# Performance work log

Hardware: AMD Instinct MI355X
Metric: run time of the kernel (lower is better)

## Reference

```python
import jax, jax.numpy as jnp
import numpy as np

D_MODEL = 1024
N_HEADS = 16
HEAD_DIM = D_MODEL // N_HEADS
D_FF = 4096
EPS = 1e-5


def _layer_norm(x, gamma, beta):
    mu = jnp.mean(x, axis=-1, keepdims=True)
    var = jnp.var(x, axis=-1, keepdims=True)
    return (x - mu) * jax.lax.rsqrt(var + EPS) * gamma + beta


def setup_inputs() -> dict:
    key = jax.random.key(0)
    ks = jax.random.split(key, 16)
    B, T, S = 2, 2048, 2048
    s = 1.0 / np.sqrt(D_MODEL)
    inp = {
        "tgt": jax.random.normal(ks[0], (B, T, D_MODEL), jnp.float32),
        "memory": jax.random.normal(ks[1], (B, S, D_MODEL), jnp.float32),
        "wq": jax.random.normal(ks[2], (D_MODEL, D_MODEL), jnp.float32) * s,
        "bq": jnp.zeros((D_MODEL,), jnp.float32),
        "wk": jax.random.normal(ks[3], (D_MODEL, D_MODEL), jnp.float32) * s,
        "bk": jnp.zeros((D_MODEL,), jnp.float32),
        "wv": jax.random.normal(ks[4], (D_MODEL, D_MODEL), jnp.float32) * s,
        "bv": jnp.zeros((D_MODEL,), jnp.float32),
        "wo": jax.random.normal(ks[5], (D_MODEL, D_MODEL), jnp.float32) * s,
        "bo": jnp.zeros((D_MODEL,), jnp.float32),
        "w1": jax.random.normal(ks[6], (D_MODEL, D_FF), jnp.float32) * s,
        "b1": jnp.zeros((D_FF,), jnp.float32),
        "w2": jax.random.normal(ks[7], (D_FF, D_MODEL), jnp.float32) * (1.0 / np.sqrt(D_FF)),
        "b2": jnp.zeros((D_MODEL,), jnp.float32),
        "g1": jnp.ones((D_MODEL,), jnp.float32),
        "be1": jnp.zeros((D_MODEL,), jnp.float32),
        "g2": jnp.ones((D_MODEL,), jnp.float32),
        "be2": jnp.zeros((D_MODEL,), jnp.float32),
    }
    return inp


def reference(tgt, memory, wq, bq, wk, bk, wv, bv, wo, bo, w1, b1, w2, b2, g1, be1, g2, be2):
    B, T, _ = tgt.shape
    S = memory.shape[1]
    scale = HEAD_DIM ** -0.5
    # projections -> [B, H, L, Dh]
    Q = (tgt @ wq + bq).reshape(B, T, N_HEADS, HEAD_DIM).transpose(0, 2, 1, 3)
    K = (memory @ wk + bk).reshape(B, S, N_HEADS, HEAD_DIM).transpose(0, 2, 1, 3)
    V = (memory @ wv + bv).reshape(B, S, N_HEADS, HEAD_DIM).transpose(0, 2, 1, 3)
    scores = jnp.einsum("bhtd,bhsd->bhts", Q, K) * scale
    attn = jax.nn.softmax(scores, axis=-1)  # dropout=0 (eval)
    ctx = jnp.einsum("bhts,bhsd->bhtd", attn, V)
    ctx = ctx.transpose(0, 2, 1, 3).reshape(B, T, D_MODEL)
    attn_out = ctx @ wo + bo
    # post-norm residual blocks
    x = _layer_norm(tgt + attn_out, g1, be1)
    ff = jax.nn.relu(x @ w1 + b1) @ w2 + b2
    out = _layer_norm(x + ff, g2, be2)
    return out
```

## Files before the change

### kernel.cpp

```cpp
#include <hip/hip_runtime.h>


typedef unsigned short u16;
typedef __attribute__((ext_vector_type(8))) short bvec8;
typedef __attribute__((ext_vector_type(4))) float fvec4;
typedef __attribute__((ext_vector_type(4))) unsigned uvec4;

#define MFMA16(a, b, c) __builtin_amdgcn_mfma_f32_16x16x32_bf16((a), (b), (c), 0, 0, 0)

__device__ __forceinline__ u16 f2b(float f) {
  union { float f; unsigned u; } x; x.f = f;
  unsigned u = x.u;
  return (u16)((u + 0x7FFFu + ((u >> 16) & 1u)) >> 16);
}
__device__ __forceinline__ unsigned cvtpk(float lo, float hi) {
  unsigned r;
  asm("v_cvt_pk_bf16_f32 %0, %1, %2" : "=v"(r) : "v"(lo), "v"(hi));
  return r;
}
#define PLSWAP32(a, b) asm("v_permlane32_swap_b32 %0, %1" : "+v"(a), "+v"(b))
#define PLSWAP16(a, b) asm("v_permlane16_swap_b32 %0, %1" : "+v"(a), "+v"(b))

__device__ __forceinline__ void gl_lds16(const u16* g, u16* lds) {
  __builtin_amdgcn_global_load_lds(
      (const __attribute__((address_space(1))) void*)g,
      (__attribute__((address_space(3))) void*)lds, 16, 0, 0);
}

__global__ __launch_bounds__(256) void k_pre(
    const float* __restrict__ tgt, const float* __restrict__ mem,
    const float* __restrict__ wq, const float* __restrict__ wk,
    const float* __restrict__ wv, const float* __restrict__ wo,
    const float* __restrict__ w1, const float* __restrict__ w2,
    u16* __restrict__ tgt_b, u16* __restrict__ mem_b,
    u16* __restrict__ wqT, u16* __restrict__ wkvT, u16* __restrict__ woT,
    u16* __restrict__ w1T, u16* __restrict__ w2T) {
  __shared__ float t[32][33];
  int bb = blockIdx.x;
  if (bb < 8192) {
    const float* in = (bb < 4096) ? tgt : mem;
    u16* outp = (bb < 4096) ? tgt_b : mem_b;
    int i = (bb & 4095) * 256 + threadIdx.x;
    float4 v = ((const float4*)in)[i];
    ushort4 o;
    o.x = f2b(v.x); o.y = f2b(v.y); o.z = f2b(v.z); o.w = f2b(v.w);
    ((ushort4*)outp)[i] = o;
    return;
  }
  int b = bb - 8192;
  const float* W; u16* WT; int K, N, bx, by;
  if (b < 4096) {
    int m = b >> 10, tt = b & 1023;
    bx = tt & 31; by = tt >> 5; K = 1024; N = 1024;
    W = (m == 0) ? wq : (m == 1) ? wk : (m == 2) ? wv : wo;
    WT = (m == 0) ? wqT : (m == 1) ? wkvT : (m == 2) ? wkvT + 1024 * 1024 : woT;
  } else if (b < 8192) {
    int tt = b - 4096; bx = tt & 127; by = tt >> 7; K = 1024; N = 4096;
    W = w1; WT = w1T;
  } else {
    int tt = b - 8192; bx = tt & 31; by = tt >> 5; K = 4096; N = 1024;
    W = w2; WT = w2T;
  }
  int tx = threadIdx.x & 31, ty = threadIdx.x >> 5;
  int n0 = bx * 32, k0 = by * 32;
#pragma unroll
  for (int i = 0; i < 4; i++)
    t[ty + i * 8][tx] = W[(size_t)(k0 + ty + i * 8) * N + n0 + tx];
  __syncthreads();
#pragma unroll
  for (int i = 0; i < 4; i++)
    WT[(size_t)(n0 + ty + i * 8) * K + k0 + tx] = f2b(t[tx][ty + i * 8]);
}

__global__ __launch_bounds__(256, 4) void k_qkv(
    const u16* __restrict__ tgt_b, const u16* __restrict__ mem_b,
    const u16* __restrict__ wqT, const u16* __restrict__ wkvT,
    const float* __restrict__ bq, const float* __restrict__ bk,
    const float* __restrict__ bv,
    u16* __restrict__ Qb, u16* __restrict__ Kb, u16* __restrict__ Vtb) {
  __shared__ u16 S[256 * 64];
  const int tid = threadIdx.x, w = tid >> 6, lane = tid & 63;
  const int q = lane >> 4, l = lane & 15;
  const bool isQ = blockIdx.x < 256;
  const int pq = isQ ? blockIdx.x : blockIdx.x - 256;
  const int lx = (pq >> 3) & (isQ ? 7 : 15);
  const int ly = (pq & 7) + ((pq >> (isQ ? 6 : 7)) << 3);
  const int m0 = ly * 128, n0 = lx * 128;
  const u16* A = isQ ? tgt_b : mem_b;
  const u16* BT = isQ ? wqT : wkvT;
  const int wm = (w >> 1) * 64, wn = (w & 1) * 64;
  const int rowin = lane >> 3, grp = lane & 7;
  const int gcol = ((grp + rowin) & 7) * 8;
  const int kc0 = ((q + 8 - (l & 7)) & 7) * 8;
  const int kc1 = ((q + 12 - (l & 7)) & 7) * 8;
  const u16* gp[8];
  u16* lp[8];
#pragma unroll
  for (int c = 0; c < 8; c++) {
    int r0 = (w * 8 + c) * 8;
    gp[c] = (r0 < 128) ? A + (size_t)(m0 + r0 + rowin) * 1024 + gcol
                       : BT + (size_t)(n0 + r0 - 128 + rowin) * 1024 + gcol;
    lp[c] = &S[r0 * 64];
  }
  fvec4 acc[4][4] = {};
#pragma unroll 1
  for (int k0 = 0; k0 < 1024; k0 += 64) {
#pragma unroll
    for (int c = 0; c < 8; c++) gl_lds16(gp[c] + k0, lp[c]);
    __syncthreads();
#pragma unroll
    for (int kh = 0; kh < 2; kh++) {
      const int kc = kh ? kc1 : kc0;
      bvec8 af[4], bf[4];
#pragma unroll
      for (int i = 0; i < 4; i++) {
        af[i] = *(const bvec8*)&S[(wm + 16 * i + l) * 64 + kc];
        bf[i] = *(const bvec8*)&S[(128 + wn + 16 * i + l) * 64 + kc];
      }
#pragma unroll
      for (int i = 0; i < 4; i++)
#pragma unroll
        for (int j = 0; j < 4; j++)
          acc[i][j] = MFMA16(af[i], bf[j], acc[i][j]);
    }
    __syncthreads();
  }
#pragma unroll
  for (int mi = 0; mi < 4; mi++)
#pragma unroll
    for (int ni = 0; ni < 4; ni++) {
      int row = m0 + wm + mi * 16 + q * 4;
      int col = n0 + wn + ni * 16 + l;
      if (isQ) {
        float bvv = bq[col];
#pragma unroll
        for (int r = 0; r < 4; r++)
          Qb[(size_t)(row + r) * 1024 + col] = f2b((acc[mi][ni][r] + bvv) * 0.125f);
      } else if (col < 1024) {
        float bvv = bk[col];
#pragma unroll
        for (int r = 0; r < 4; r++)
          Kb[(size_t)(row + r) * 1024 + col] = f2b(acc[mi][ni][r] + bvv);
      } else {
        int vcol = col - 1024;
        float bvv = bv[vcol];
        int b = row >> 11, s = row & 2047;
        int h = vcol >> 6, d = vcol & 63;
        ushort4 o;
        o.x = f2b(acc[mi][ni][0] + bvv);
        o.y = f2b(acc[mi][ni][1] + bvv);
        o.z = f2b(acc[mi][ni][2] + bvv);
        o.w = f2b(acc[mi][ni][3] + bvv);
        *(ushort4*)&Vtb[((size_t)(b * 16 + h) * 64 + d) * 2048 + s] = o;
      }
    }
}

template <int TM, int TN>
__global__ __launch_bounds__(256, 4) void k_gemm(
    const u16* __restrict__ A, const u16* __restrict__ BT,
    const float* __restrict__ bias, const float* __restrict__ resid,
    float* __restrict__ outF, u16* __restrict__ outB,
    int M, int N, int Kstride, int Klen, float scale, int flags) {
  constexpr int WM = TM / 2, WN = TN / 2;
  constexpr int MI = WM / 16, NI = WN / 16;
  constexpr int NCALL = (TM + TN) / 32;
  __shared__ u16 S[(TM + TN) * 64];
  const int tid = threadIdx.x, w = tid >> 6, lane = tid & 63;
  const int q = lane >> 4, l = lane & 15;
  const int nx = gridDim.x, nyh = gridDim.y >> 3;
  const int p = blockIdx.x + nx * (blockIdx.y + gridDim.y * blockIdx.z);
  const int q8 = p >> 3;
  const int lx = q8 & (nx - 1);
  const int t = q8 >> __builtin_ctz(nx);
  const int ly = (p & 7) + ((t & (nyh - 1)) << 3);
  const int lz = t >> __builtin_ctz(nyh);
  const int m0 = ly * TM, n0 = lx * TN;
  const int kbeg = lz * Klen;
  const int wm = (w >> 1) * WM, wn = (w & 1) * WN;
  const int rowin = lane >> 3, grp = lane & 7;
  const int gcol = ((grp + rowin) & 7) * 8;
  const int kc0 = ((q + 8 - (l & 7)) & 7) * 8;
  const int kc1 = ((q + 12 - (l & 7)) & 7) * 8;
  const u16* gp[NCALL];
  u16* lp[NCALL];
#pragma unroll
  for (int c = 0; c < NCALL; c++) {
    int r0 = (w * NCALL + c) * 8;
    gp[c] = (r0 < TM) ? A + (size_t)(m0 + r0 + rowin) * Kstride + kbeg + gcol
                      : BT + (size_t)(n0 + r0 - TM + rowin) * Kstride + kbeg + gcol;
    lp[c] = &S[r0 * 64];
  }
  fvec4 acc[MI][NI] = {};
#pragma unroll 1
  for (int k0 = 0; k0 < Klen; k0 += 64) {
#pragma unroll
    for (int c = 0; c < NCALL; c++) gl_lds16(gp[c] + k0, lp[c]);
    __syncthreads();
#pragma unroll
    for (int kh = 0; kh < 2; kh++) {
      const int kc = kh ? kc1 : kc0;
      bvec8 af[MI], bf[NI];
#pragma unroll
      for (int i = 0; i < MI; i++)
        af[i] = *(const bvec8*)&S[(wm + 16 * i + l) * 64 + kc];
#pragma unroll
      for (int j = 0; j < NI; j++)
        bf[j] = *(const bvec8*)&S[(TM + wn + 16 * j + l) * 64 + kc];
#pragma unroll
      for (int i = 0; i < MI; i++)
#pragma unroll
        for (int j = 0; j < NI; j++)
          acc[i][j] = MFMA16(af[i], bf[j], acc[i][j]);
    }
    __syncthreads();
  }
  if (flags & 16) {
    float* po = outF + (size_t)lz * M * N;
#pragma unroll
    for (int mi = 0; mi < MI; mi++)
#pragma unroll
      for (int ni = 0; ni < NI; ni++) {
        int row = m0 + wm + mi * 16 + q * 4;
        int col = n0 + wn + ni * 16 + l;
#pragma unroll
        for (int r = 0; r < 4; r++)
          po[(size_t)(row + r) * N + col] = acc[mi][ni][r];
      }
    return;
  }
#pragma unroll
  for (int mi = 0; mi < MI; mi++)
#pragma unroll
    for (int ni = 0; ni < NI; ni++) {
      int row = m0 + wm + mi * 16 + q * 4;
      int col = n0 + wn + ni * 16 + l;
      float bvv = bias[col];
#pragma unroll
      for (int r = 0; r < 4; r++) {
        float v = (acc[mi][ni][r] + bvv) * scale;
        if (flags & 1) v = fmaxf(v, 0.0f);
        size_t idx = (size_t)(row + r) * N + col;
        if (flags & 8) v += resid[idx];
        if (flags & 2) outB[idx] = f2b(v);
        if (flags & 4) outF[idx] = v;
      }
    }
}

__global__ __launch_bounds__(256, 4) void k_attn(
    const u16* __restrict__ Q, const u16* __restrict__ Kb,
    const u16* __restrict__ Vt, float* __restrict__ opart,
    float* __restrict__ lpart) {
  __shared__ u16 Ks[2][64 * 64];
  __shared__ u16 Vs[2][64 * 64];
  const int tid = threadIdx.x, w = tid >> 6, lane = tid & 63;
  const int q = lane >> 4, l = lane & 15;
  const int bx = blockIdx.x;
  const int blk = (bx & 7) * 64 + (bx >> 3);
  const int bh = blk >> 4, tb = blk & 15;
  const int b = bh >> 4, h = bh & 15;
  const int t0 = tb * 128 + w * 32;
  const int sbeg = blockIdx.y * 1024;
  float* op = opart + (size_t)blockIdx.y * 4096 * 1024;
  float* lp = lpart + (size_t)blockIdx.y * 4096 * 16;
  const u16* Qp = Q + (size_t)(b * 2048 + t0) * 1024 + h * 64;
  const u16* Kp = Kb + (size_t)(b * 2048) * 1024 + h * 64;
  const u16* Vp = Vt + (size_t)bh * 64 * 2048;
  const int rowin = lane >> 3, grp = lane & 7;
  const int gcol = ((grp + rowin) & 7) * 8;
  const int kc0 = ((q + 8 - (l & 7)) & 7) * 8;
  const int kc1 = ((q + 12 - (l & 7)) & 7) * 8;
  bvec8 aQ[2][2];
#pragma unroll
  for (int ti = 0; ti < 2; ti++)
#pragma unroll
    for (int kh = 0; kh < 2; kh++)
      aQ[ti][kh] = *(const bvec8*)&Qp[(size_t)(ti * 16 + l) * 1024 + kh * 32 + q * 8];
  const short oneb = (short)0x3F80;
  const bvec8 aOne = {oneb, oneb, oneb, oneb, oneb, oneb, oneb, oneb};
  fvec4 o[2][4] = {};
  fvec4 lacc[2] = {};
  auto stage = [&](int bb, int sv) {
    gl_lds16(Kp + (size_t)(sv + w * 8 + rowin) * 1024 + gcol, &Ks[bb][(w * 8) * 64]);
    gl_lds16(Kp + (size_t)(sv + 32 + w * 8 + rowin) * 1024 + gcol, &Ks[bb][(32 + w * 8) * 64]);
    gl_lds16(Vp + (size_t)(w * 8 + rowin) * 2048 + sv + gcol, &Vs[bb][(w * 8) * 64]);
    gl_lds16(Vp + (size_t)(32 + w * 8 + rowin) * 2048 + sv + gcol, &Vs[bb][(32 + w * 8) * 64]);
  };
  stage(0, sbeg);
  int cur = 0;
#pragma unroll 1
  for (int s0 = sbeg; s0 < sbeg + 1024; s0 += 64) {
    __syncthreads();
    if (s0 + 64 < sbeg + 1024) stage(cur ^ 1, s0 + 64);
    const u16* KsC = Ks[cur];
    const u16* VsC = Vs[cur];
    unsigned pw[2][4][2];
    __builtin_amdgcn_s_setprio(1);
#pragma unroll
    for (int ss = 0; ss < 4; ss++) {
      const int ro = (ss * 16 + l) * 64;
      bvec8 kf0 = *(const bvec8*)&KsC[ro + kc0];
      bvec8 kf1 = *(const bvec8*)&KsC[ro + kc1];
#pragma unroll
      for (int ti = 0; ti < 2; ti++) {
        fvec4 sc = {0.f, 0.f, 0.f, 0.f};
        sc = MFMA16(kf0, aQ[ti][0], sc);
        sc = MFMA16(kf1, aQ[ti][1], sc);
        float p0 = __expf(sc[0]), p1 = __expf(sc[1]);
        float p2 = __expf(sc[2]), p3 = __expf(sc[3]);
        pw[ti][ss][0] = cvtpk(p0, p1);
        pw[ti][ss][1] = cvtpk(p2, p3);
      }
    }
    __builtin_amdgcn_s_setprio(0);
#pragma unroll
    for (int ti = 0; ti < 2; ti++)
#pragma unroll
      for (int b4 = 0; b4 < 2; b4++)
#pragma unroll
        for (int r2 = 0; r2 < 2; r2++) {
          PLSWAP32(pw[ti][2 * b4][r2], pw[ti][2 * b4 + 1][r2]);
          PLSWAP16(pw[ti][2 * b4][r2], pw[ti][2 * b4 + 1][r2]);
        }
    bvec8 bP[2][2];
#pragma unroll
    for (int ti = 0; ti < 2; ti++)
#pragma unroll
      for (int kh = 0; kh < 2; kh++) {
        uvec4 t = {pw[ti][2 * kh][0], pw[ti][2 * kh][1],
                   pw[ti][2 * kh + 1][0], pw[ti][2 * kh + 1][1]};
        bP[ti][kh] = __builtin_bit_cast(bvec8, t);
      }
    bvec8 bV[4][2];
#pragma unroll
    for (int dt = 0; dt < 4; dt++) {
      const int ro = (dt * 16 + l) * 64;
      bV[dt][0] = *(const bvec8*)&VsC[ro + kc0];
      bV[dt][1] = *(const bvec8*)&VsC[ro + kc1];
    }
    __builtin_amdgcn_s_setprio(1);
#pragma unroll
    for (int dt = 0; dt < 4; dt++)
#pragma unroll
      for (int ti = 0; ti < 2; ti++) {
        o[ti][dt] = MFMA16(bV[dt][0], bP[ti][0], o[ti][dt]);
        o[ti][dt] = MFMA16(bV[dt][1], bP[ti][1], o[ti][dt]);
      }
#pragma unroll
    for (int ti = 0; ti < 2; ti++) {
      lacc[ti] = MFMA16(aOne, bP[ti][0], lacc[ti]);
      lacc[ti] = MFMA16(aOne, bP[ti][1], lacc[ti]);
    }
    __builtin_amdgcn_s_setprio(0);
    cur ^= 1;
  }
#pragma unroll
  for (int ti = 0; ti < 2; ti++) {
    int trow = b * 2048 + t0 + ti * 16 + l;
    if (q == 0) lp[trow * 16 + h] = lacc[ti][0];
#pragma unroll
    for (int dt = 0; dt < 4; dt++)
      *(fvec4*)&op[(size_t)trow * 1024 + h * 64 + dt * 16 + q * 4] = o[ti][dt];
  }
}

__global__ __launch_bounds__(256) void k_actx(const float* __restrict__ opart,
                                              const float* __restrict__ lpart,
                                              u16* __restrict__ ctx) {
  int row = blockIdx.x, c0 = threadIdx.x * 4;
  int h = c0 >> 6;
  float lsum = lpart[row * 16 + h] + lpart[4096 * 16 + row * 16 + h];
  float inv = 1.0f / lsum;
  float4 a = *(const float4*)&opart[(size_t)row * 1024 + c0];
  float4 b = *(const float4*)&opart[(size_t)4096 * 1024 + (size_t)row * 1024 + c0];
  ushort4 o;
  o.x = f2b((a.x + b.x) * inv);
  o.y = f2b((a.y + b.y) * inv);
  o.z = f2b((a.z + b.z) * inv);
  o.w = f2b((a.w + b.w) * inv);
  *(ushort4*)&ctx[(size_t)row * 1024 + c0] = o;
}

__global__ __launch_bounds__(256) void k_lnp(
    const float* __restrict__ parts, int nparts,
    const float* __restrict__ bias, const float* __restrict__ resid,
    const float* __restrict__ g, const float* __restrict__ be,
    float* __restrict__ xf, u16* __restrict__ xb) {
  __shared__ float sm[8];
  int row = blockIdx.x, tid = threadIdx.x;
  size_t base = (size_t)row * 1024;
  const size_t pstride = (size_t)4096 * 1024;
  float v[4], s = 0.f, ss = 0.f;
#pragma unroll
  for (int j = 0; j < 4; j++) {
    int c = tid + j * 256;
    float acc = bias[c] + resid[base + c];
    for (int z = 0; z < nparts; z++) acc += parts[z * pstride + base + c];
    v[j] = acc;
    s += acc; ss += acc * acc;
  }
#pragma unroll
  for (int off = 32; off; off >>= 1) {
    s += __shfl_down(s, off, 64);
    ss += __shfl_down(ss, off, 64);
  }
  int w = tid >> 6;
  if ((tid & 63) == 0) { sm[w] = s; sm[4 + w] = ss; }
  __syncthreads();
  float S = sm[0] + sm[1] + sm[2] + sm[3];
  float SS = sm[4] + sm[5] + sm[6] + sm[7];
  float mean = S * (1.0f / 1024.0f);
  float var = SS * (1.0f / 1024.0f) - mean * mean;
  float rstd = rsqrtf(var + 1e-5f);
#pragma unroll
  for (int j = 0; j < 4; j++) {
    int c = tid + j * 256;
    float o = (v[j] - mean) * rstd * g[c] + be[c];
    xf[base + c] = o;
    if (xb) xb[base + c] = f2b(o);
  }
}

extern "C" void kernel_launch(void* const* d_in, const int* in_sizes, int n_in,
                              void* d_out, int out_size, void* d_ws, size_t ws_size,
                              hipStream_t stream) {
  (void)in_sizes; (void)n_in; (void)out_size; (void)ws_size;
  const float* tgt = (const float*)d_in[0];
  const float* mem = (const float*)d_in[1];
  const float* wq  = (const float*)d_in[2];
  const float* bq  = (const float*)d_in[3];
  const float* wk  = (const float*)d_in[4];
  const float* bk  = (const float*)d_in[5];
  const float* wv  = (const float*)d_in[6];
  const float* bv  = (const float*)d_in[7];
  const float* wo  = (const float*)d_in[8];
  const float* bo  = (const float*)d_in[9];
  const float* w1  = (const float*)d_in[10];
  const float* b1  = (const float*)d_in[11];
  const float* w2  = (const float*)d_in[12];
  const float* b2  = (const float*)d_in[13];
  const float* g1  = (const float*)d_in[14];
  const float* be1 = (const float*)d_in[15];
  const float* g2  = (const float*)d_in[16];
  const float* be2 = (const float*)d_in[17];
  float* out = (float*)d_out;

  char* ws = (char*)d_ws;
  size_t off = 0;
  auto take = [&](size_t bytes) { char* p = ws + off; off += bytes; return p; };
  const size_t MB = 1024 * 1024;
  u16* tgt_b = (u16*)take(8 * MB);
  u16* mem_b = (u16*)take(8 * MB);
  u16* wqT   = (u16*)take(2 * MB);
  u16* wkvT  = (u16*)take(4 * MB);
  u16* woT   = (u16*)take(2 * MB);
  u16* w1T   = (u16*)take(8 * MB);
  u16* w2T   = (u16*)take(8 * MB);
  u16* Qb    = (u16*)take(8 * MB);
  u16* Kb    = (u16*)take(8 * MB);
  u16* Vtb   = (u16*)take(8 * MB);
  u16* ctx   = (u16*)take(8 * MB);
  float* opart = (float*)take(32 * MB);
  float* opj   = (float*)take(32 * MB);
  float* lpart = (float*)take(1 * MB);
  float* xf  = (float*)take(16 * MB);
  u16* xb    = (u16*)take(8 * MB);
  u16* hbuf  = Qb;
  float* fp2 = opart;

  k_pre<<<20480, 256, 0, stream>>>(tgt, mem, wq, wk, wv, wo, w1, w2,
                                   tgt_b, mem_b, wqT, wkvT, woT, w1T, w2T);
  k_qkv<<<768, 256, 0, stream>>>(tgt_b, mem_b, wqT, wkvT, bq, bk, bv,
                                 Qb, Kb, Vtb);
  k_attn<<<dim3(512, 2), 256, 0, stream>>>(Qb, Kb, Vtb, opart, lpart);
  k_actx<<<4096, 256, 0, stream>>>(opart, lpart, ctx);
  k_gemm<64, 128><<<dim3(8, 64, 1), 256, 0, stream>>>(
      ctx, woT, nullptr, nullptr, opj, nullptr,
      4096, 1024, 1024, 1024, 1.0f, 16);
  k_lnp<<<4096, 256, 0, stream>>>(opj, 1, bo, tgt, g1, be1, xf, xb);
  k_gemm<128, 128><<<dim3(32, 32), 256, 0, stream>>>(
      xb, w1T, b1, nullptr, nullptr, hbuf,
      4096, 4096, 1024, 1024, 1.0f, 1 | 2);
  k_gemm<64, 128><<<dim3(8, 64, 2), 256, 0, stream>>>(
      hbuf, w2T, nullptr, nullptr, fp2, nullptr,
      4096, 1024, 4096, 2048, 1.0f, 16);
  k_lnp<<<4096, 256, 0, stream>>>(fp2, 2, b2, xf, g2, be2, out, nullptr);
}
```

Measured before the change: 370.7 us.

## Drop split-KV attention; normalize and emit bf16 context inside attention kernel

Attention previously split the key sequence into two halves across blockIdx.y, wrote fp32 partial outputs and row sums, then ran a separate combine kernel. Each block now covers the full 2048 keys for 64 query rows (16 per wave instead of 32), normalizes by the row sum and writes bf16 ctx directly. This removes the 32MB fp32 partial write/read and one launch. In exchange, K/V tiles are reused across half as many query rows per block, so K/V LDS traffic per unit of work doubles. Each loop iteration also does half as much MFMA work between barriers.

```diff
diff --git a/kernel.cpp b/kernel.cpp
--- a/kernel.cpp
+++ b/kernel.cpp
@@ -250,20 +250,16 @@
 
 __global__ __launch_bounds__(256, 4) void k_attn(
     const u16* __restrict__ Q, const u16* __restrict__ Kb,
-    const u16* __restrict__ Vt, float* __restrict__ opart,
-    float* __restrict__ lpart) {
+    const u16* __restrict__ Vt, u16* __restrict__ ctx) {
   __shared__ u16 Ks[2][64 * 64];
   __shared__ u16 Vs[2][64 * 64];
   const int tid = threadIdx.x, w = tid >> 6, lane = tid & 63;
   const int q = lane >> 4, l = lane & 15;
   const int bx = blockIdx.x;
-  const int blk = (bx & 7) * 64 + (bx >> 3);
-  const int bh = blk >> 4, tb = blk & 15;
+  const int blk = (bx & 7) * 128 + (bx >> 3);
+  const int bh = blk >> 5, tb = blk & 31;
   const int b = bh >> 4, h = bh & 15;
-  const int t0 = tb * 128 + w * 32;
-  const int sbeg = blockIdx.y * 1024;
-  float* op = opart + (size_t)blockIdx.y * 4096 * 1024;
-  float* lp = lpart + (size_t)blockIdx.y * 4096 * 16;
+  const int t0 = tb * 64 + w * 16;
   const u16* Qp = Q + (size_t)(b * 2048 + t0) * 1024 + h * 64;
   const u16* Kp = Kb + (size_t)(b * 2048) * 1024 + h * 64;
   const u16* Vp = Vt + (size_t)bh * 64 * 2048;
@@ -271,67 +267,58 @@
   const int gcol = ((grp + rowin) & 7) * 8;
   const int kc0 = ((q + 8 - (l & 7)) & 7) * 8;
   const int kc1 = ((q + 12 - (l & 7)) & 7) * 8;
-  bvec8 aQ[2][2];
-#pragma unroll
-  for (int ti = 0; ti < 2; ti++)
-#pragma unroll
-    for (int kh = 0; kh < 2; kh++)
-      aQ[ti][kh] = *(const bvec8*)&Qp[(size_t)(ti * 16 + l) * 1024 + kh * 32 + q * 8];
+  bvec8 aQ[2];
+#pragma unroll
+  for (int kh = 0; kh < 2; kh++)
+    aQ[kh] = *(const bvec8*)&Qp[(size_t)l * 1024 + kh * 32 + q * 8];
   const short oneb = (short)0x3F80;
   const bvec8 aOne = {oneb, oneb, oneb, oneb, oneb, oneb, oneb, oneb};
-  fvec4 o[2][4] = {};
-  fvec4 lacc[2] = {};
+  fvec4 o[4] = {};
+  fvec4 lacc = {};
   auto stage = [&](int bb, int sv) {
     gl_lds16(Kp + (size_t)(sv + w * 8 + rowin) * 1024 + gcol, &Ks[bb][(w * 8) * 64]);
     gl_lds16(Kp + (size_t)(sv + 32 + w * 8 + rowin) * 1024 + gcol, &Ks[bb][(32 + w * 8) * 64]);
     gl_lds16(Vp + (size_t)(w * 8 + rowin) * 2048 + sv + gcol, &Vs[bb][(w * 8) * 64]);
     gl_lds16(Vp + (size_t)(32 + w * 8 + rowin) * 2048 + sv + gcol, &Vs[bb][(32 + w * 8) * 64]);
   };
-  stage(0, sbeg);
+  stage(0, 0);
   int cur = 0;
 #pragma unroll 1
-  for (int s0 = sbeg; s0 < sbeg + 1024; s0 += 64) {
+  for (int s0 = 0; s0 < 2048; s0 += 64) {
     __syncthreads();
-    if (s0 + 64 < sbeg + 1024) stage(cur ^ 1, s0 + 64);
+    if (s0 + 64 < 2048) stage(cur ^ 1, s0 + 64);
     const u16* KsC = Ks[cur];
     const u16* VsC = Vs[cur];
-    unsigned pw[2][4][2];
+    unsigned pw[4][2];
     __builtin_amdgcn_s_setprio(1);
 #pragma unroll
     for (int ss = 0; ss < 4; ss++) {
       const int ro = (ss * 16 + l) * 64;
       bvec8 kf0 = *(const bvec8*)&KsC[ro + kc0];
       bvec8 kf1 = *(const bvec8*)&KsC[ro + kc1];
-#pragma unroll
-      for (int ti = 0; ti < 2; ti++) {
-        fvec4 sc = {0.f, 0.f, 0.f, 0.f};
-        sc = MFMA16(kf0, aQ[ti][0], sc);
-        sc = MFMA16(kf1, aQ[ti][1], sc);
-        float p0 = __expf(sc[0]), p1 = __expf(sc[1]);
-        float p2 = __expf(sc[2]), p3 = __expf(sc[3]);
-        pw[ti][ss][0] = cvtpk(p0, p1);
-        pw[ti][ss][1] = cvtpk(p2, p3);
+      fvec4 sc = {0.f, 0.f, 0.f, 0.f};
+      sc = MFMA16(kf0, aQ[0], sc);
+      sc = MFMA16(kf1, aQ[1], sc);
+      float p0 = __expf(sc[0]), p1 = __expf(sc[1]);
+      float p2 = __expf(sc[2]), p3 = __expf(sc[3]);
+      pw[ss][0] = cvtpk(p0, p1);
+      pw[ss][1] = cvtpk(p2, p3);
+    }
+    __builtin_amdgcn_s_setprio(0);
+#pragma unroll
+    for (int b4 = 0; b4 < 2; b4++)
+#pragma unroll
+      for (int r2 = 0; r2 < 2; r2++) {
+        PLSWAP32(pw[2 * b4][r2], pw[2 * b4 + 1][r2]);
+        PLSWAP16(pw[2 * b4][r2], pw[2 * b4 + 1][r2]);
       }
-    }
-    __builtin_amdgcn_s_setprio(0);
-#pragma unroll
-    for (int ti = 0; ti < 2; ti++)
-#pragma unroll
-      for (int b4 = 0; b4 < 2; b4++)
-#pragma unroll
-        for (int r2 = 0; r2 < 2; r2++) {
-          PLSWAP32(pw[ti][2 * b4][r2], pw[ti][2 * b4 + 1][r2]);
-          PLSWAP16(pw[ti][2 * b4][r2], pw[ti][2 * b4 + 1][r2]);
-        }
-    bvec8 bP[2][2];
-#pragma unroll
-    for (int ti = 0; ti < 2; ti++)
-#pragma unroll
-      for (int kh = 0; kh < 2; kh++) {
-        uvec4 t = {pw[ti][2 * kh][0], pw[ti][2 * kh][1],
-                   pw[ti][2 * kh + 1][0], pw[ti][2 * kh + 1][1]};
-        bP[ti][kh] = __builtin_bit_cast(bvec8, t);
-      }
+    bvec8 bP[2];
+#pragma unroll
+    for (int kh = 0; kh < 2; kh++) {
+      uvec4 t = {pw[2 * kh][0], pw[2 * kh][1],
+                 pw[2 * kh + 1][0], pw[2 * kh + 1][1]};
+      bP[kh] = __builtin_bit_cast(bvec8, t);
+    }
     bvec8 bV[4][2];
 #pragma unroll
     for (int dt = 0; dt < 4; dt++) {
@@ -341,45 +328,26 @@
     }
     __builtin_amdgcn_s_setprio(1);
 #pragma unroll
-    for (int dt = 0; dt < 4; dt++)
-#pragma unroll
-      for (int ti = 0; ti < 2; ti++) {
-        o[ti][dt] = MFMA16(bV[dt][0], bP[ti][0], o[ti][dt]);
-        o[ti][dt] = MFMA16(bV[dt][1], bP[ti][1], o[ti][dt]);
-      }
-#pragma unroll
-    for (int ti = 0; ti < 2; ti++) {
-      lacc[ti] = MFMA16(aOne, bP[ti][0], lacc[ti]);
-      lacc[ti] = MFMA16(aOne, bP[ti][1], lacc[ti]);
-    }
+    for (int dt = 0; dt < 4; dt++) {
+      o[dt] = MFMA16(bV[dt][0], bP[0], o[dt]);
+      o[dt] = MFMA16(bV[dt][1], bP[1], o[dt]);
+    }
+    lacc = MFMA16(aOne, bP[0], lacc);
+    lacc = MFMA16(aOne, bP[1], lacc);
     __builtin_amdgcn_s_setprio(0);
     cur ^= 1;
   }
-#pragma unroll
-  for (int ti = 0; ti < 2; ti++) {
-    int trow = b * 2048 + t0 + ti * 16 + l;
-    if (q == 0) lp[trow * 16 + h] = lacc[ti][0];
-#pragma unroll
-    for (int dt = 0; dt < 4; dt++)
-      *(fvec4*)&op[(size_t)trow * 1024 + h * 64 + dt * 16 + q * 4] = o[ti][dt];
-  }
-}
-
-__global__ __launch_bounds__(256) void k_actx(const float* __restrict__ opart,
-                                              const float* __restrict__ lpart,
-                                              u16* __restrict__ ctx) {
-  int row = blockIdx.x, c0 = threadIdx.x * 4;
-  int h = c0 >> 6;
-  float lsum = lpart[row * 16 + h] + lpart[4096 * 16 + row * 16 + h];
-  float inv = 1.0f / lsum;
-  float4 a = *(const float4*)&opart[(size_t)row * 1024 + c0];
-  float4 b = *(const float4*)&opart[(size_t)4096 * 1024 + (size_t)row * 1024 + c0];
-  ushort4 o;
-  o.x = f2b((a.x + b.x) * inv);
-  o.y = f2b((a.y + b.y) * inv);
-  o.z = f2b((a.z + b.z) * inv);
-  o.w = f2b((a.w + b.w) * inv);
-  *(ushort4*)&ctx[(size_t)row * 1024 + c0] = o;
+  const float inv = 1.0f / lacc[0];
+  u16* cp = ctx + (size_t)(b * 2048 + t0 + l) * 1024 + h * 64;
+#pragma unroll
+  for (int dt = 0; dt < 4; dt++) {
+    ushort4 o4;
+    o4.x = f2b(o[dt][0] * inv);
+    o4.y = f2b(o[dt][1] * inv);
+    o4.z = f2b(o[dt][2] * inv);
+    o4.w = f2b(o[dt][3] * inv);
+    *(ushort4*)&cp[dt * 16 + q * 4] = o4;
+  }
 }
 
 __global__ __launch_bounds__(256) void k_lnp(
@@ -461,20 +429,17 @@
   u16* Kb    = (u16*)take(8 * MB);
   u16* Vtb   = (u16*)take(8 * MB);
   u16* ctx   = (u16*)take(8 * MB);
-  float* opart = (float*)take(32 * MB);
+  float* fp2   = (float*)take(32 * MB);
   float* opj   = (float*)take(32 * MB);
-  float* lpart = (float*)take(1 * MB);
   float* xf  = (float*)take(16 * MB);
   u16* xb    = (u16*)take(8 * MB);
   u16* hbuf  = Qb;
-  float* fp2 = opart;
 
   k_pre<<<20480, 256, 0, stream>>>(tgt, mem, wq, wk, wv, wo, w1, w2,
                                    tgt_b, mem_b, wqT, wkvT, woT, w1T, w2T);
   k_qkv<<<768, 256, 0, stream>>>(tgt_b, mem_b, wqT, wkvT, bq, bk, bv,
                                  Qb, Kb, Vtb);
-  k_attn<<<dim3(512, 2), 256, 0, stream>>>(Qb, Kb, Vtb, opart, lpart);
-  k_actx<<<4096, 256, 0, stream>>>(opart, lpart, ctx);
+  k_attn<<<1024, 256, 0, stream>>>(Qb, Kb, Vtb, ctx);
   k_gemm<64, 128><<<dim3(8, 64, 1), 256, 0, stream>>>(
       ctx, woT, nullptr, nullptr, opj, nullptr,
       4096, 1024, 1024, 1024, 1.0f, 16);
```

Measured after the change: 367.7 us. About the same (-0.8%).

## Drop split-S attention and fuse normalization into attention epilogue

Applied to the files above, without the earlier changes.

The attention kernel no longer splits the key dimension across two grid slices. Each block now iterates over all 2048 keys and normalizes its output by the row sum directly, writing bf16 context. This removes the fp32 partial-output round trip and the separate combine kernel. The exponential is also replaced with a raw v_exp_f32 on a log2e-scaled input. The trade-off is half as many blocks (512) and a serial loop twice as long, which lowers parallelism on a GPU with many CUs.

```diff
diff --git a/kernel.cpp b/kernel.cpp
--- a/kernel.cpp
+++ b/kernel.cpp
@@ -7,11 +7,17 @@
 typedef __attribute__((ext_vector_type(4))) unsigned uvec4;
 
 #define MFMA16(a, b, c) __builtin_amdgcn_mfma_f32_16x16x32_bf16((a), (b), (c), 0, 0, 0)
+#define LOG2E 1.44269504088896f
 
 __device__ __forceinline__ u16 f2b(float f) {
   union { float f; unsigned u; } x; x.f = f;
   unsigned u = x.u;
   return (u16)((u + 0x7FFFu + ((u >> 16) & 1u)) >> 16);
+}
+__device__ __forceinline__ float ex2(float x) {
+  float r;
+  asm("v_exp_f32 %0, %1" : "=v"(r) : "v"(x));
+  return r;
 }
 __device__ __forceinline__ unsigned cvtpk(float lo, float hi) {
   unsigned r;
@@ -250,8 +256,7 @@
 
 __global__ __launch_bounds__(256, 4) void k_attn(
     const u16* __restrict__ Q, const u16* __restrict__ Kb,
-    const u16* __restrict__ Vt, float* __restrict__ opart,
-    float* __restrict__ lpart) {
+    const u16* __restrict__ Vt, u16* __restrict__ ctx) {
   __shared__ u16 Ks[2][64 * 64];
   __shared__ u16 Vs[2][64 * 64];
   const int tid = threadIdx.x, w = tid >> 6, lane = tid & 63;
@@ -261,9 +266,6 @@
   const int bh = blk >> 4, tb = blk & 15;
   const int b = bh >> 4, h = bh & 15;
   const int t0 = tb * 128 + w * 32;
-  const int sbeg = blockIdx.y * 1024;
-  float* op = opart + (size_t)blockIdx.y * 4096 * 1024;
-  float* lp = lpart + (size_t)blockIdx.y * 4096 * 16;
   const u16* Qp = Q + (size_t)(b * 2048 + t0) * 1024 + h * 64;
   const u16* Kp = Kb + (size_t)(b * 2048) * 1024 + h * 64;
   const u16* Vp = Vt + (size_t)bh * 64 * 2048;
@@ -287,12 +289,12 @@
     gl_lds16(Vp + (size_t)(w * 8 + rowin) * 2048 + sv + gcol, &Vs[bb][(w * 8) * 64]);
     gl_lds16(Vp + (size_t)(32 + w * 8 + rowin) * 2048 + sv + gcol, &Vs[bb][(32 + w * 8) * 64]);
   };
-  stage(0, sbeg);
+  stage(0, 0);
   int cur = 0;
 #pragma unroll 1
-  for (int s0 = sbeg; s0 < sbeg + 1024; s0 += 64) {
+  for (int s0 = 0; s0 < 2048; s0 += 64) {
     __syncthreads();
-    if (s0 + 64 < sbeg + 1024) stage(cur ^ 1, s0 + 64);
+    if (s0 + 64 < 2048) stage(cur ^ 1, s0 + 64);
     const u16* KsC = Ks[cur];
     const u16* VsC = Vs[cur];
     unsigned pw[2][4][2];
@@ -307,8 +309,8 @@
         fvec4 sc = {0.f, 0.f, 0.f, 0.f};
         sc = MFMA16(kf0, aQ[ti][0], sc);
         sc = MFMA16(kf1, aQ[ti][1], sc);
-        float p0 = __expf(sc[0]), p1 = __expf(sc[1]);
-        float p2 = __expf(sc[2]), p3 = __expf(sc[3]);
+        float p0 = ex2(sc[0] * LOG2E), p1 = ex2(sc[1] * LOG2E);
+        float p2 = ex2(sc[2] * LOG2E), p3 = ex2(sc[3] * LOG2E);
         pw[ti][ss][0] = cvtpk(p0, p1);
         pw[ti][ss][1] = cvtpk(p2, p3);
       }
@@ -357,29 +359,18 @@
   }
 #pragma unroll
   for (int ti = 0; ti < 2; ti++) {
-    int trow = b * 2048 + t0 + ti * 16 + l;
-    if (q == 0) lp[trow * 16 + h] = lacc[ti][0];
-#pragma unroll
-    for (int dt = 0; dt < 4; dt++)
-      *(fvec4*)&op[(size_t)trow * 1024 + h * 64 + dt * 16 + q * 4] = o[ti][dt];
-  }
-}
-
-__global__ __launch_bounds__(256) void k_actx(const float* __restrict__ opart,
-                                              const float* __restrict__ lpart,
-                                              u16* __restrict__ ctx) {
-  int row = blockIdx.x, c0 = threadIdx.x * 4;
-  int h = c0 >> 6;
-  float lsum = lpart[row * 16 + h] + lpart[4096 * 16 + row * 16 + h];
-  float inv = 1.0f / lsum;
-  float4 a = *(const float4*)&opart[(size_t)row * 1024 + c0];
-  float4 b = *(const float4*)&opart[(size_t)4096 * 1024 + (size_t)row * 1024 + c0];
-  ushort4 o;
-  o.x = f2b((a.x + b.x) * inv);
-  o.y = f2b((a.y + b.y) * inv);
-  o.z = f2b((a.z + b.z) * inv);
-  o.w = f2b((a.w + b.w) * inv);
-  *(ushort4*)&ctx[(size_t)row * 1024 + c0] = o;
+    const float inv = 1.0f / lacc[ti][0];
+    u16* cp = ctx + (size_t)(b * 2048 + t0 + ti * 16 + l) * 1024 + h * 64;
+#pragma unroll
+    for (int dt = 0; dt < 4; dt++) {
+      ushort4 o4;
+      o4.x = f2b(o[ti][dt][0] * inv);
+      o4.y = f2b(o[ti][dt][1] * inv);
+      o4.z = f2b(o[ti][dt][2] * inv);
+      o4.w = f2b(o[ti][dt][3] * inv);
+      *(ushort4*)&cp[dt * 16 + q * 4] = o4;
+    }
+  }
 }
 
 __global__ __launch_bounds__(256) void k_lnp(
@@ -461,20 +452,17 @@
   u16* Kb    = (u16*)take(8 * MB);
   u16* Vtb   = (u16*)take(8 * MB);
   u16* ctx   = (u16*)take(8 * MB);
-  float* opart = (float*)take(32 * MB);
+  float* fp2   = (float*)take(32 * MB);
   float* opj   = (float*)take(32 * MB);
-  float* lpart = (float*)take(1 * MB);
   float* xf  = (float*)take(16 * MB);
   u16* xb    = (u16*)take(8 * MB);
   u16* hbuf  = Qb;
-  float* fp2 = opart;
 
   k_pre<<<20480, 256, 0, stream>>>(tgt, mem, wq, wk, wv, wo, w1, w2,
                                    tgt_b, mem_b, wqT, wkvT, woT, w1T, w2T);
   k_qkv<<<768, 256, 0, stream>>>(tgt_b, mem_b, wqT, wkvT, bq, bk, bv,
                                  Qb, Kb, Vtb);
-  k_attn<<<dim3(512, 2), 256, 0, stream>>>(Qb, Kb, Vtb, opart, lpart);
-  k_actx<<<4096, 256, 0, stream>>>(opart, lpart, ctx);
+  k_attn<<<512, 256, 0, stream>>>(Qb, Kb, Vtb, ctx);
   k_gemm<64, 128><<<dim3(8, 64, 1), 256, 0, stream>>>(
       ctx, woT, nullptr, nullptr, opj, nullptr,
       4096, 1024, 1024, 1024, 1.0f, 16);
```

Result: faster. 358.2 us (-3.4%).
